# Kernel tuning notes

Measured on AMD Instinct MI355X. Metric: run time of the kernel, lower is better.

## Reference

```python
import jax, jax.numpy as jnp
import numpy as np

B, N, DIM = 2, 2048, 1024
H, DH = 16, 64
INNER = H * DH            # 1024
FF_INNER = 4 * DIM        # 4096
EPS = 1e-5


def _layer_norm(x, g, b):
    mu = jnp.mean(x, axis=-1, keepdims=True)
    var = jnp.mean(jnp.square(x - mu), axis=-1, keepdims=True)
    return (x - mu) * jax.lax.rsqrt(var + EPS) * g + b


def _self_attention(x, wq, wk, wv, wo, bo):
    # wq/wk/wv: [INNER, DIM] (torch Linear layout, y = x @ W^T)
    b, n, _ = x.shape
    q = jnp.einsum('bnd,id->bni', x, wq).reshape(b, n, H, DH).transpose(0, 2, 1, 3)
    k = jnp.einsum('bnd,id->bni', x, wk).reshape(b, n, H, DH).transpose(0, 2, 1, 3)
    v = jnp.einsum('bnd,id->bni', x, wv).reshape(b, n, H, DH).transpose(0, 2, 1, 3)
    scale = DH ** -0.5
    sim = jnp.einsum('bhid,bhjd->bhij', q, k) * scale   # [B,H,N,N]
    attn = jax.nn.softmax(sim, axis=-1)
    out = jnp.einsum('bhij,bhjd->bhid', attn, v)
    out = out.transpose(0, 2, 1, 3).reshape(b, n, INNER)
    return jnp.einsum('bni,di->bnd', out, wo) + bo


def _geglu_ff(x, w1, b1, w2, b2):
    # w1: [2*FF_INNER, DIM], w2: [DIM, FF_INNER]
    h = jnp.einsum('bnd,id->bni', x, w1) + b1
    a, gate = jnp.split(h, 2, axis=-1)
    h = a * jax.nn.gelu(gate, approximate=False)
    return jnp.einsum('bni,di->bnd', h, w2) + b2


def setup_inputs() -> dict:
    key = jax.random.key(0)
    ks = jax.random.split(key, 12)
    s = 0.02
    inp = {
        'x': jax.random.normal(ks[0], (B, N, DIM), jnp.float32),
        'ln1_g': jnp.ones((DIM,), jnp.float32),
        'ln1_b': jnp.zeros((DIM,), jnp.float32),
        'w_q1': jax.random.normal(ks[1], (INNER, DIM), jnp.float32) * s,
        'w_k1': jax.random.normal(ks[2], (INNER, DIM), jnp.float32) * s,
        'w_v1': jax.random.normal(ks[3], (INNER, DIM), jnp.float32) * s,
        'w_o1': jax.random.normal(ks[4], (DIM, INNER), jnp.float32) * s,
        'b_o1': jnp.zeros((DIM,), jnp.float32),
        'ln2_g': jnp.ones((DIM,), jnp.float32),
        'ln2_b': jnp.zeros((DIM,), jnp.float32),
        'w_q2': jax.random.normal(ks[5], (INNER, DIM), jnp.float32) * s,
        'w_k2': jax.random.normal(ks[6], (INNER, DIM), jnp.float32) * s,
        'w_v2': jax.random.normal(ks[7], (INNER, DIM), jnp.float32) * s,
        'w_o2': jax.random.normal(ks[8], (DIM, INNER), jnp.float32) * s,
        'b_o2': jnp.zeros((DIM,), jnp.float32),
        'ln3_g': jnp.ones((DIM,), jnp.float32),
        'ln3_b': jnp.zeros((DIM,), jnp.float32),
        'w_ff1': jax.random.normal(ks[9], (2 * FF_INNER, DIM), jnp.float32) * s,
        'b_ff1': jnp.zeros((2 * FF_INNER,), jnp.float32),
        'w_ff2': jax.random.normal(ks[10], (DIM, FF_INNER), jnp.float32) * s,
        'b_ff2': jnp.zeros((DIM,), jnp.float32),
    }
    return inp


def reference(x, ln1_g, ln1_b, w_q1, w_k1, w_v1, w_o1, b_o1,
              ln2_g, ln2_b, w_q2, w_k2, w_v2, w_o2, b_o2,
              ln3_g, ln3_b, w_ff1, b_ff1, w_ff2, b_ff2):
    # attn1 (self) + residual
    x = _self_attention(_layer_norm(x, ln1_g, ln1_b), w_q1, w_k1, w_v1, w_o1, b_o1) + x
    # attn2 (self, context=None) + residual
    x = _self_attention(_layer_norm(x, ln2_g, ln2_b), w_q2, w_k2, w_v2, w_o2, b_o2) + x
    # GEGLU feed-forward + residual
    x = _geglu_ff(_layer_norm(x, ln3_g, ln3_b), w_ff1, b_ff1, w_ff2, b_ff2) + x
    return x
```

## Files before the change

### kernel.cpp

```cpp
#include <hip/hip_runtime.h>
#include <hip/hip_bf16.h>

using bf16x8 = __attribute__((ext_vector_type(8))) short;
using f32x4  = __attribute__((ext_vector_type(4))) float;
using f32x16 = __attribute__((ext_vector_type(16))) float;
typedef unsigned int u32;
typedef unsigned short u16;
using u32x4 = __attribute__((ext_vector_type(4))) u32;

__device__ __forceinline__ u16 f2b(float f) {
  union { float f; u32 u; } v; v.f = f;
  return (u16)((v.u + 0x7FFFu + ((v.u >> 16) & 1u)) >> 16);
}

__device__ __forceinline__ u32 cvtpk(float lo, float hi) {
  u32 r;
  asm("v_cvt_pk_bf16_f32 %0, %1, %2" : "=v"(r) : "v"(lo), "v"(hi));
  return r;
}

__device__ __forceinline__ float exp2_raw(float x) {
  float r;
  asm("v_exp_f32 %0, %1" : "=v"(r) : "v"(x));
  return r;
}

__device__ __forceinline__ void gload16(const void* g, void* l) {
  __builtin_amdgcn_global_load_lds((const __attribute__((address_space(1))) u32*)g,
                                   (__attribute__((address_space(3))) u32*)l, 16, 0, 0);
}

__device__ __forceinline__ float gelu_fast(float x) {
  const float x2 = x * x;
  const float t = x * fmaf(0.044715f, x2, 1.f);
  const float u = exp2f(2.3022080f * t);
  return x * u * __builtin_amdgcn_rcpf(u + 1.f);
}

__global__ __launch_bounds__(256) void castall(
    const float* __restrict__ wq1, const float* __restrict__ wk1,
    const float* __restrict__ wv1, const float* __restrict__ wo1,
    const float* __restrict__ wq2, const float* __restrict__ wk2,
    const float* __restrict__ wv2, const float* __restrict__ wo2,
    const float* __restrict__ wff1, const float* __restrict__ wff2,
    u16* __restrict__ qkv1, u16* __restrict__ o1,
    u16* __restrict__ qkv2, u16* __restrict__ o2,
    u16* __restrict__ ff1p, u16* __restrict__ ff2) {
  const long e = ((long)blockIdx.x * 256 + threadIdx.x) * 4;
  constexpr long M1 = 1l << 20;
  const float* s; u16* d;
  if (e < 3 * M1) {
    s = (e < M1 ? wq1 + e : (e < 2 * M1 ? wk1 + (e - M1) : wv1 + (e - 2 * M1)));
    d = qkv1 + e;
  } else if (e < 4 * M1) {
    s = wo1 + (e - 3 * M1); d = o1 + (e - 3 * M1);
  } else if (e < 7 * M1) {
    long r = e - 4 * M1;
    s = (r < M1 ? wq2 + r : (r < 2 * M1 ? wk2 + (r - M1) : wv2 + (r - 2 * M1)));
    d = qkv2 + r;
  } else if (e < 8 * M1) {
    s = wo2 + (e - 7 * M1); d = o2 + (e - 7 * M1);
  } else if (e < 16 * M1) {
    long r = e - 8 * M1;
    long p = r >> 10, col = r & 1023;
    long g = p >> 5, rr = p & 31;
    long lr = (rr < 16) ? (g << 4) + rr : 4096 + (g << 4) + (rr - 16);
    s = wff1 + (lr << 10) + col; d = ff1p + r;
  } else {
    long r = e - 16 * M1;
    s = wff2 + r; d = ff2 + r;
  }
  float4 v = *(const float4*)s;
  ushort4 o;
  o.x = f2b(v.x); o.y = f2b(v.y); o.z = f2b(v.z); o.w = f2b(v.w);
  *(ushort4*)d = o;
}

__global__ __launch_bounds__(256) void ln_kernel(const float* __restrict__ x,
                                                 const float* __restrict__ g,
                                                 const float* __restrict__ b,
                                                 u16* __restrict__ y) {
  const int row = blockIdx.x;
  const int t = threadIdx.x;
  const float* xr = x + (size_t)row * 1024;
  float4 v = ((const float4*)xr)[t];
  float s  = v.x + v.y + v.z + v.w;
  float s2 = v.x * v.x + v.y * v.y + v.z * v.z + v.w * v.w;
  #pragma unroll
  for (int m = 1; m < 64; m <<= 1) {
    s  += __shfl_xor(s, m);
    s2 += __shfl_xor(s2, m);
  }
  __shared__ float red[8];
  if ((t & 63) == 0) { red[(t >> 6) * 2] = s; red[(t >> 6) * 2 + 1] = s2; }
  __syncthreads();
  s  = red[0] + red[2] + red[4] + red[6];
  s2 = red[1] + red[3] + red[5] + red[7];
  const float mu = s * (1.f / 1024.f);
  const float var = s2 * (1.f / 1024.f) - mu * mu;
  const float rs = rsqrtf(var + 1e-5f);
  float4 gv = ((const float4*)g)[t];
  float4 bv = ((const float4*)b)[t];
  ushort4 o;
  o.x = f2b((v.x - mu) * rs * gv.x + bv.x);
  o.y = f2b((v.y - mu) * rs * gv.y + bv.y);
  o.z = f2b((v.z - mu) * rs * gv.z + bv.z);
  o.w = f2b((v.w - mu) * rs * gv.w + bv.w);
  ((ushort4*)(y + (size_t)row * 1024))[t] = o;
}

__global__ __launch_bounds__(512, 4) void gemm_out(
    const u16* __restrict__ A, const u16* __restrict__ Bw,
    const float* __restrict__ bias, const float* __restrict__ resid,
    float* __restrict__ out, int N, int K) {
  extern __shared__ u16 lds[];
  const int tid = threadIdx.x;
  const int l = tid & 63, wid = tid >> 6;
  const int li = l & 15, lg = l >> 4;
  const int wr = wid >> 2, wc = wid & 3;
  const int nx = N >> 7;
  const int cpx = gridDim.x >> 3;
  const int v = (blockIdx.x & 7) * cpx + (blockIdx.x >> 3);
  const int by = v / nx, bx = v - by * nx;
  const int m0 = by << 7, n0 = bx << 7;

  const int sr = tid >> 3;
  const int sc = ((tid & 7) ^ (sr & 7)) << 3;
  const int dc = (tid & 7) << 3;
  const int sc0 = (lg * 8) ^ ((li & 7) << 3);
  const int sc1 = sc0 ^ 32;

  f32x4 acc[4][2] = {};

  auto stageA = [&](int kb, int t2) {
    #pragma unroll
    for (int s = 0; s < 2; ++s)
      gload16(A + (size_t)(m0 + s * 64 + sr) * K + t2 * 64 + sc,
              lds + kb * 8192 + (s * 64 + sr) * 64 + dc);
  };
  auto stageB = [&](int kb, int t2) {
    #pragma unroll
    for (int s = 0; s < 2; ++s)
      gload16(Bw + (size_t)(n0 + s * 64 + sr) * K + t2 * 64 + sc,
              lds + 16384 + kb * 8192 + (s * 64 + sr) * 64 + dc);
  };

  const int NT = K >> 6;
  stageA(0, 0); stageB(0, 0);
  __builtin_amdgcn_sched_barrier(0);
  stageA(1, 1); stageB(1, 1);
  __builtin_amdgcn_sched_barrier(0);
  asm volatile("s_waitcnt vmcnt(4)" ::: "memory");
  __builtin_amdgcn_s_barrier();
  __builtin_amdgcn_sched_barrier(0);

  for (int t = 0; t < NT; ++t) {
    const int kb = t & 1;
    const u16* Ab = lds + kb * 8192 + (wr * 64 + li) * 64;
    const u16* Bb = lds + 16384 + kb * 8192 + (wc * 32 + li) * 64;
    bf16x8 a[4], b[2];

    #pragma unroll
    for (int mi = 0; mi < 4; ++mi) a[mi] = *(const bf16x8*)(Ab + mi * 1024 + sc0);
    #pragma unroll
    for (int n = 0; n < 2; ++n)  b[n]  = *(const bf16x8*)(Bb + n * 1024 + sc0);
    __builtin_amdgcn_s_barrier();
    __builtin_amdgcn_s_setprio(1);
    #pragma unroll
    for (int mi = 0; mi < 4; ++mi)
      #pragma unroll
      for (int n = 0; n < 2; ++n)
        acc[mi][n] = __builtin_amdgcn_mfma_f32_16x16x32_bf16(a[mi], b[n], acc[mi][n], 0, 0, 0);
    __builtin_amdgcn_s_setprio(0);
    __builtin_amdgcn_s_barrier();

    #pragma unroll
    for (int mi = 0; mi < 4; ++mi) a[mi] = *(const bf16x8*)(Ab + mi * 1024 + sc1);
    #pragma unroll
    for (int n = 0; n < 2; ++n)  b[n]  = *(const bf16x8*)(Bb + n * 1024 + sc1);
    __builtin_amdgcn_s_barrier();
    __builtin_amdgcn_s_setprio(1);
    #pragma unroll
    for (int mi = 0; mi < 4; ++mi)
      #pragma unroll
      for (int n = 0; n < 2; ++n)
        acc[mi][n] = __builtin_amdgcn_mfma_f32_16x16x32_bf16(a[mi], b[n], acc[mi][n], 0, 0, 0);
    __builtin_amdgcn_s_setprio(0);
    if (t + 2 < NT) {
      stageA(kb, t + 2); stageB(kb, t + 2);
      asm volatile("s_waitcnt vmcnt(4)" ::: "memory");
    } else if (t + 2 == NT) {
      asm volatile("s_waitcnt vmcnt(0)" ::: "memory");
    }
    __builtin_amdgcn_s_barrier();
    __builtin_amdgcn_sched_barrier(0);
  }

  #pragma unroll
  for (int mi = 0; mi < 4; ++mi) {
    const int m = m0 + wr * 64 + mi * 16 + lg * 4;
    #pragma unroll
    for (int n = 0; n < 2; ++n) {
      const int j = n0 + wc * 32 + n * 16 + li;
      const float bj = bias[j];
      #pragma unroll
      for (int rb = 0; rb < 4; ++rb)
        out[(size_t)(m + rb) * N + j] =
            acc[mi][n][rb] + bj + resid[(size_t)(m + rb) * N + j];
    }
  }
}

#define KLOOP_PROLOGUE()                                                      \
  stageA(0, 0); stageB(0, 0); stageA(1, 0); stageB(1, 0);                     \
  __builtin_amdgcn_sched_barrier(0);                                          \
  stageA(0, 1); stageB(0, 1);                                                 \
  __builtin_amdgcn_sched_barrier(0);                                          \
  asm volatile("s_waitcnt vmcnt(4)" ::: "memory");                            \
  __builtin_amdgcn_s_barrier();                                               \
  __builtin_amdgcn_sched_barrier(0);

#define KLOOP_BODY(NT)                                                        \
  bf16x8 b0[4], b1[4];                                                        \
  for (int t = 0; t < NT; ++t) {                                              \
    const int kb = t & 1;                                                     \
    const u16* Abase0 = lds + (kb * 2 + 0) * 8192 + rowA0;                    \
    const u16* Abase1 = lds + (kb * 2 + 1) * 8192 + rowA0;                    \
    const u16* Bbase  = lds + (kb * 2 + bhn) * 8192 + rowB0;                  \
    bf16x8 a[4];                                                              \
                                                      \
    _Pragma("unroll")                                                         \
    for (int j = 0; j < 4; ++j) a[j]  = *(const bf16x8*)(Abase0 + j * 1024 + sc0); \
    _Pragma("unroll")                                                         \
    for (int n = 0; n < 4; ++n) b0[n] = *(const bf16x8*)(Bbase + n * 1024 + sc0); \
    if (t + 1 < NT) stageA(1, t + 1);                                         \
    __builtin_amdgcn_s_setprio(1);                                            \
    _Pragma("unroll")                                                         \
    for (int j = 0; j < 4; ++j)                                               \
      _Pragma("unroll")                                                       \
      for (int n = 0; n < 4; ++n)                                             \
        acc[j][n] = __builtin_amdgcn_mfma_f32_16x16x32_bf16(a[j], b0[n], acc[j][n], 0, 0, 0); \
    __builtin_amdgcn_s_setprio(0);                                            \
    __builtin_amdgcn_s_barrier();                                             \
                                                      \
    _Pragma("unroll")                                                         \
    for (int j = 0; j < 4; ++j) a[j]  = *(const bf16x8*)(Abase0 + j * 1024 + sc1); \
    _Pragma("unroll")                                                         \
    for (int n = 0; n < 4; ++n) b1[n] = *(const bf16x8*)(Bbase + n * 1024 + sc1); \
    if (t + 1 < NT) stageB(1, t + 1);                                         \
    __builtin_amdgcn_s_setprio(1);                                            \
    _Pragma("unroll")                                                         \
    for (int j = 0; j < 4; ++j)                                               \
      _Pragma("unroll")                                                       \
      for (int n = 0; n < 4; ++n)                                             \
        acc[j][n] = __builtin_amdgcn_mfma_f32_16x16x32_bf16(a[j], b1[n], acc[j][n], 0, 0, 0); \
    __builtin_amdgcn_s_setprio(0);                                            \
    __builtin_amdgcn_s_barrier();                                             \
                                                      \
    _Pragma("unroll")                                                         \
    for (int j = 0; j < 4; ++j) a[j] = *(const bf16x8*)(Abase1 + j * 1024 + sc0); \
    if (t + 2 < NT) stageA(0, t + 2);                                         \
    __builtin_amdgcn_s_setprio(1);                                            \
    _Pragma("unroll")                                                         \
    for (int j = 0; j < 4; ++j)                                               \
      _Pragma("unroll")                                                       \
      for (int n = 0; n < 4; ++n)                                             \
        acc[4 + j][n] = __builtin_amdgcn_mfma_f32_16x16x32_bf16(a[j], b0[n], acc[4 + j][n], 0, 0, 0); \
    __builtin_amdgcn_s_setprio(0);                                            \
    __builtin_amdgcn_s_barrier();                                             \
                                                      \
    _Pragma("unroll")                                                         \
    for (int j = 0; j < 4; ++j) a[j] = *(const bf16x8*)(Abase1 + j * 1024 + sc1); \
    if (t + 2 < NT) stageB(0, t + 2);                                         \
    __builtin_amdgcn_s_setprio(1);                                            \
    _Pragma("unroll")                                                         \
    for (int j = 0; j < 4; ++j)                                               \
      _Pragma("unroll")                                                       \
      for (int n = 0; n < 4; ++n)                                             \
        acc[4 + j][n] = __builtin_amdgcn_mfma_f32_16x16x32_bf16(a[j], b1[n], acc[4 + j][n], 0, 0, 0); \
    __builtin_amdgcn_s_setprio(0);                                            \
    if (t < NT - 2)       asm volatile("s_waitcnt vmcnt(4)" ::: "memory");    \
    else if (t == NT - 2) asm volatile("s_waitcnt vmcnt(0)" ::: "memory");    \
    __builtin_amdgcn_s_barrier();                                             \
  }

__global__ __launch_bounds__(512, 2) void gemm_ff1(
    const u16* __restrict__ A, const u16* __restrict__ Wp,
    const float* __restrict__ bias, u16* __restrict__ out) {
  extern __shared__ u16 lds[];
  const int tid = threadIdx.x;
  const int l = tid & 63, wid = tid >> 6;
  const int li = l & 15, lg = l >> 4;
  const int wr = wid >> 2, wc = wid & 3;
  const int xcd = blockIdx.x & 7, r = blockIdx.x >> 3;
  const int bx = (xcd & 3) * 8 + (r >> 3);
  const int by = (xcd >> 2) * 8 + (r & 7);

  const int lr8 = l >> 3;
  const int scb = ((l & 7) ^ lr8) << 3;
  const int sc0 = (lg * 8) ^ ((li & 7) << 3);
  const int sc1 = sc0 ^ 32;

  const int rowA0 = (wr * 64 + li) * 64;
  const int rowB0 = 32768 + ((wc & 1) * 64 + li) * 64;
  const int bhn = wc >> 1;

  f32x4 acc[8][4] = {};

  auto stageA = [&](int h, int t2) {
    const int kb2 = t2 & 1;
    #pragma unroll
    for (int s = 0; s < 2; ++s) {
      const u16* g = A + (size_t)(by * 256 + s * 128 + h * 64 + wid * 8 + lr8) * 1024
                       + t2 * 64 + scb;
      u16* d = lds + (kb2 * 2 + h) * 8192 + s * 4096 + wid * 512;
      gload16(g, d);
    }
  };
  auto stageB = [&](int h, int t2) {
    const int kb2 = t2 & 1;
    #pragma unroll
    for (int s = 0; s < 2; ++s) {
      const u16* g = Wp + (size_t)(bx * 256 + h * 128 + s * 64 + wid * 8 + lr8) * 1024
                        + t2 * 64 + scb;
      u16* d = lds + 32768 + (kb2 * 2 + h) * 8192 + s * 4096 + wid * 512;
      gload16(g, d);
    }
  };

  KLOOP_PROLOGUE()
  KLOOP_BODY(16)

  #pragma unroll
  for (int nj = 0; nj < 2; ++nj) {
    const int c = bx * 128 + wc * 32 + nj * 16 + li;
    const float ba = bias[c];
    const float bg = bias[4096 + c];
    #pragma unroll
    for (int mi = 0; mi < 8; ++mi) {
      #pragma unroll
      for (int rb = 0; rb < 4; ++rb) {
        const float av = acc[mi][2 * nj][rb] + ba;
        const float gv = acc[mi][2 * nj + 1][rb] + bg;
        out[(size_t)(by * 256 + wr * 128 + mi * 16 + lg * 4 + rb) * 4096 + c]
            = f2b(av * gelu_fast(gv));
      }
    }
  }
}

__global__ __launch_bounds__(512, 2) void gemm_qkv(
    const u16* __restrict__ A, const u16* __restrict__ Wp,
    u16* __restrict__ outp) {
  extern __shared__ u16 lds[];
  const int tid = threadIdx.x;
  const int l = tid & 63, wid = tid >> 6;
  const int li = l & 15, lg = l >> 4;
  const int wr = wid >> 2, wc = wid & 3;
  const int xcd = blockIdx.x & 7, r = blockIdx.x >> 3;
  const int by = (xcd >> 1) * 4 + r / 6;
  const int bx = (xcd & 1) * 6 + r % 6;

  const int lr8 = l >> 3;
  const int scb = ((l & 7) ^ lr8) << 3;
  const int sc0 = (lg * 8) ^ ((li & 7) << 3);
  const int sc1 = sc0 ^ 32;

  const int rowA0 = (wr * 64 + li) * 64;
  const int rowB0 = 32768 + ((wc & 1) * 64 + li) * 64;
  const int bhn = wc >> 1;

  f32x4 acc[8][4] = {};

  auto stageA = [&](int h, int t2) {
    const int kb2 = t2 & 1;
    #pragma unroll
    for (int s = 0; s < 2; ++s) {
      const u16* g = A + (size_t)(by * 256 + s * 128 + h * 64 + wid * 8 + lr8) * 1024
                       + t2 * 64 + scb;
      u16* d = lds + (kb2 * 2 + h) * 8192 + s * 4096 + wid * 512;
      gload16(g, d);
    }
  };
  auto stageB = [&](int h, int t2) {
    const int kb2 = t2 & 1;
    #pragma unroll
    for (int s = 0; s < 2; ++s) {
      const u16* g = Wp + (size_t)(bx * 256 + h * 128 + s * 64 + wid * 8 + lr8) * 1024
                        + t2 * 64 + scb;
      u16* d = lds + 32768 + (kb2 * 2 + h) * 8192 + s * 4096 + wid * 512;
      gload16(g, d);
    }
  };

  KLOOP_PROLOGUE()
  KLOOP_BODY(16)

  #pragma unroll
  for (int mi = 0; mi < 8; ++mi) {
    const int mbase = by * 256 + wr * 128 + mi * 16 + lg * 4;
    #pragma unroll
    for (int ni = 0; ni < 4; ++ni) {
      const int j = bx * 256 + wc * 64 + ni * 16 + li;
      f32x4 a = acc[mi][ni];
      const int sec = j >> 10, jj = j & 1023;
      const int h = jj >> 6, dd = jj & 63;
      u16* base = outp + (size_t)sec * 4194304;
      if (sec == 0) {
        #pragma unroll
        for (int rb = 0; rb < 4; ++rb) {
          const int m = mbase + rb;
          const int bb = m >> 11, n = m & 2047;
          base[(((size_t)bb * 16 + h) * 2048 + n) * 64 + dd] =
              f2b(a[rb] * 0.18033688011112042f);
        }
      } else if (sec == 1) {
        #pragma unroll
        for (int rb = 0; rb < 4; ++rb) {
          const int m = mbase + rb;
          const int bb = m >> 11, n = m & 2047;
          base[(((size_t)bb * 16 + h) * 2048 + n) * 64 + (dd ^ ((n & 7) << 3))] =
              f2b(a[rb]);
        }
      } else {
        const int bb = mbase >> 11, n = mbase & 2047;
        const int ng = n & ~63, nl = n & 63;
        const int nl2 = (nl & 51) | ((nl & 4) << 1) | ((nl & 8) >> 1);
        const int col = ng | (nl2 ^ ((dd & 7) << 3));
        ushort4 pk;
        pk.x = f2b(a[0]); pk.y = f2b(a[1]); pk.z = f2b(a[2]); pk.w = f2b(a[3]);
        *(ushort4*)&base[(((size_t)bb * 16 + h) * 64 + dd) * 2048 + col] = pk;
      }
    }
  }
}

__global__ __launch_bounds__(256, 2) void attn_fwd(
    const u16* __restrict__ Q, const u16* __restrict__ K,
    const u16* __restrict__ Vt, u16* __restrict__ Out) {
  __shared__ u16 smem[3][8192];
  const int tid = threadIdx.x;
  const int l = tid & 63, w = tid >> 6;
  const int lo = l & 31, hi = l >> 5, l7 = l & 7;
  const int bh = blockIdx.x & 31, qt = blockIdx.x >> 5;
  const int b_ = bh >> 4, h = bh & 15;

  const u16* Qg = Q + ((size_t)bh * 2048 + qt * 128 + w * 32 + lo) * 64;
  const u16* Kg = K + (size_t)bh * 2048 * 64;
  const u16* Vg = Vt + (size_t)bh * 64 * 2048;

  bf16x8 qf[4];
  #pragma unroll
  for (int d = 0; d < 4; ++d) qf[d] = *(const bf16x8*)&Qg[d * 16 + hi * 8];

  f32x16 o0 = {}, o1 = {};
  float lrow = 0.f;

  auto stage = [&](int buf, int jt) {
    #pragma unroll
    for (int i = 0; i < 2; ++i)
      gload16(Kg + (size_t)jt * 4096 + i * 2048 + tid * 8,
              &smem[buf][i * 2048 + w * 512]);
    #pragma unroll
    for (int i = 0; i < 2; ++i)
      gload16(Vg + (size_t)(w * 8 + (l >> 3) + i * 32) * 2048 + jt * 64 + l7 * 8,
              &smem[buf][4096 + i * 2048 + w * 512]);
  };

  __builtin_amdgcn_sched_barrier(0);
  stage(0, 0);
  __builtin_amdgcn_sched_barrier(0);
  stage(1, 1);
  __builtin_amdgcn_sched_barrier(0);

  int cur = 0, pre = 2;
  for (int jt = 0; jt < 32; ++jt) {
    if (jt == 0)      asm volatile("s_waitcnt vmcnt(8)" ::: "memory");
    else if (jt < 31) asm volatile("s_waitcnt vmcnt(4)" ::: "memory");
    else              asm volatile("s_waitcnt vmcnt(0)" ::: "memory");
    __builtin_amdgcn_s_barrier();
    __builtin_amdgcn_sched_barrier(0);
    if (jt + 2 < 32) stage(pre, jt + 2);

    const u16* Kl = &smem[cur][0];
    const u16* Vl = &smem[cur][4096];

    bf16x8 kf[4][2], vf0[4], vf1[4];
    #pragma unroll
    for (int dc = 0; dc < 4; ++dc) {
      const int col = (dc * 16 + hi * 8) ^ (l7 << 3);
      kf[dc][0] = *(const bf16x8*)&Kl[lo * 64 + col];
      kf[dc][1] = *(const bf16x8*)&Kl[(32 + lo) * 64 + col];
      vf0[dc]   = *(const bf16x8*)&Vl[lo * 64 + col];
      vf1[dc]   = *(const bf16x8*)&Vl[(32 + lo) * 64 + col];
    }

    f32x16 st[2] = {};
    __builtin_amdgcn_s_setprio(1);
    #pragma unroll
    for (int dc = 0; dc < 4; ++dc) {
      st[0] = __builtin_amdgcn_mfma_f32_32x32x16_bf16(kf[dc][0], qf[dc], st[0], 0, 0, 0);
      st[1] = __builtin_amdgcn_mfma_f32_32x32x16_bf16(kf[dc][1], qf[dc], st[1], 0, 0, 0);
    }
    __builtin_amdgcn_s_setprio(0);

    float p[32], sm[16];
    #pragma unroll
    for (int r = 0; r < 16; ++r) p[r]      = exp2_raw(st[0][r] - 8.f);
    #pragma unroll
    for (int r = 0; r < 16; ++r) p[16 + r] = exp2_raw(st[1][r] - 8.f);
    #pragma unroll
    for (int r = 0; r < 16; ++r) sm[r] = p[r] + p[16 + r];
    #pragma unroll
    for (int s2 = 8; s2 >= 1; s2 >>= 1)
      #pragma unroll
      for (int r = 0; r < s2; ++r) sm[r] += sm[r + s2];
    lrow += sm[0] + __shfl_xor(sm[0], 32);

    bf16x8 pf[4];
    #pragma unroll
    for (int kp = 0; kp < 4; ++kp) {
      u32x4 wv;
      #pragma unroll
      for (int t2 = 0; t2 < 4; ++t2)
        wv[t2] = cvtpk(p[(kp >> 1) * 16 + (kp & 1) * 8 + t2 * 2],
                       p[(kp >> 1) * 16 + (kp & 1) * 8 + t2 * 2 + 1]);
      union { u32x4 a; bf16x8 b; } cc; cc.a = wv;
      pf[kp] = cc.b;
    }

    __builtin_amdgcn_s_setprio(1);
    #pragma unroll
    for (int kp = 0; kp < 4; ++kp) {
      o0 = __builtin_amdgcn_mfma_f32_32x32x16_bf16(vf0[kp], pf[kp], o0, 0, 0, 0);
      o1 = __builtin_amdgcn_mfma_f32_32x32x16_bf16(vf1[kp], pf[kp], o1, 0, 0, 0);
    }
    __builtin_amdgcn_s_setprio(0);

    cur = (cur == 2) ? 0 : cur + 1;
    pre = (pre == 2) ? 0 : pre + 1;
  }

  const float inv = 1.f / lrow;
  u16* Ob = Out + ((size_t)b_ * 2048 + qt * 128 + w * 32 + lo) * 1024 + h * 64;
  #pragma unroll
  for (int dd = 0; dd < 2; ++dd) {
    #pragma unroll
    for (int R = 0; R < 4; ++R) {
      ushort4 pk;
      const f32x16 oo = dd ? o1 : o0;
      pk.x = f2b(oo[4 * R + 0] * inv); pk.y = f2b(oo[4 * R + 1] * inv);
      pk.z = f2b(oo[4 * R + 2] * inv); pk.w = f2b(oo[4 * R + 3] * inv);
      *(ushort4*)&Ob[dd * 32 + 8 * R + 4 * hi] = pk;
    }
  }
}

extern "C" void kernel_launch(void* const* d_in, const int* in_sizes, int n_in,
                              void* d_out, int out_size, void* d_ws, size_t ws_size,
                              hipStream_t stream) {
  const float* x    = (const float*)d_in[0];
  const float* ln1g = (const float*)d_in[1];
  const float* ln1b = (const float*)d_in[2];
  const float* wq1  = (const float*)d_in[3];
  const float* wk1  = (const float*)d_in[4];
  const float* wv1  = (const float*)d_in[5];
  const float* wo1  = (const float*)d_in[6];
  const float* bo1  = (const float*)d_in[7];
  const float* ln2g = (const float*)d_in[8];
  const float* ln2b = (const float*)d_in[9];
  const float* wq2  = (const float*)d_in[10];
  const float* wk2  = (const float*)d_in[11];
  const float* wv2  = (const float*)d_in[12];
  const float* wo2  = (const float*)d_in[13];
  const float* bo2  = (const float*)d_in[14];
  const float* ln3g = (const float*)d_in[15];
  const float* ln3b = (const float*)d_in[16];
  const float* wff1 = (const float*)d_in[17];
  const float* bff1 = (const float*)d_in[18];
  const float* wff2 = (const float*)d_in[19];
  const float* bff2 = (const float*)d_in[20];

  char* ws = (char*)d_ws;
  const size_t MB = 1024 * 1024;
  u16* wqkv1b = (u16*)(ws + 0 * MB);
  u16* wo1b   = (u16*)(ws + 6 * MB);
  u16* wqkv2b = (u16*)(ws + 8 * MB);
  u16* wo2b   = (u16*)(ws + 14 * MB);
  u16* wff1p  = (u16*)(ws + 16 * MB);
  u16* wff2b  = (u16*)(ws + 32 * MB);
  u16* xn     = (u16*)(ws + 40 * MB);
  u16* Qb     = (u16*)(ws + 48 * MB);
  float* x1   = (float*)(ws + 72 * MB);
  float* x2   = (float*)(ws + 88 * MB);
  u16* hact   = (u16*)(ws + 48 * MB);
  u16* Kb  = Qb + 4194304;
  u16* Vtb = Qb + 8388608;

  hipFuncSetAttribute((const void*)gemm_ff1,
                      hipFuncAttributeMaxDynamicSharedMemorySize, 131072);
  hipFuncSetAttribute((const void*)gemm_qkv,
                      hipFuncAttributeMaxDynamicSharedMemorySize, 131072);
  hipFuncSetAttribute((const void*)gemm_out,
                      hipFuncAttributeMaxDynamicSharedMemorySize, 65536);

  castall<<<20480, 256, 0, stream>>>(wq1, wk1, wv1, wo1, wq2, wk2, wv2, wo2,
                                     wff1, wff2,
                                     wqkv1b, wo1b, wqkv2b, wo2b, wff1p, wff2b);

  ln_kernel<<<4096, 256, 0, stream>>>(x, ln1g, ln1b, xn);
  gemm_qkv<<<192, 512, 131072, stream>>>(xn, wqkv1b, Qb);
  attn_fwd<<<512, 256, 0, stream>>>(Qb, Kb, Vtb, xn);
  gemm_out<<<256, 512, 65536, stream>>>(xn, wo1b, bo1, x, x1, 1024, 1024);

  ln_kernel<<<4096, 256, 0, stream>>>(x1, ln2g, ln2b, xn);
  gemm_qkv<<<192, 512, 131072, stream>>>(xn, wqkv2b, Qb);
  attn_fwd<<<512, 256, 0, stream>>>(Qb, Kb, Vtb, xn);
  gemm_out<<<256, 512, 65536, stream>>>(xn, wo2b, bo2, x1, x2, 1024, 1024);

  ln_kernel<<<4096, 256, 0, stream>>>(x2, ln3g, ln3b, xn);
  gemm_ff1<<<512, 512, 131072, stream>>>(xn, wff1p, bff1, hact);
  gemm_out<<<256, 512, 65536, stream>>>(hact, wff2b, bff2, x2, (float*)d_out, 1024, 4096);
}
```

Baseline: 357.7 us.

## Split attention over two key halves and merge partials in a combine kernel

The attention kernel now splits each (batch, head, query-tile) over two halves of the key sequence. This doubles the grid to 1024 blocks, raises the launch-bounds occupancy target to 4, and shrinks the LDS ring from three buffers to two with full waits. Each half writes unnormalized bf16 partial outputs and row sums to workspace. A new combine kernel adds the two partials, normalizes them and scatters the result into the head-interleaved layout. The aim is better CU occupancy and parallelism. The cost is an extra launch, extra global traffic for the partials, bf16 rounding of the intermediate partials, and a shallower prefetch pipeline.

```diff
diff --git a/kernel.cpp b/kernel.cpp
--- a/kernel.cpp
+++ b/kernel.cpp
@@ -11,6 +11,11 @@
 __device__ __forceinline__ u16 f2b(float f) {
   union { float f; u32 u; } v; v.f = f;
   return (u16)((v.u + 0x7FFFu + ((v.u >> 16) & 1u)) >> 16);
+}
+
+__device__ __forceinline__ float b2f(u16 b) {
+  union { u32 u; float f; } v; v.u = ((u32)b) << 16;
+  return v.f;
 }
 
 __device__ __forceinline__ u32 cvtpk(float lo, float hi) {
@@ -435,15 +440,16 @@
   }
 }
 
-__global__ __launch_bounds__(256, 2) void attn_fwd(
+__global__ __launch_bounds__(256, 4) void attn_split(
     const u16* __restrict__ Q, const u16* __restrict__ K,
-    const u16* __restrict__ Vt, u16* __restrict__ Out) {
-  __shared__ u16 smem[3][8192];
+    const u16* __restrict__ Vt, u16* __restrict__ Op, float* __restrict__ Lp) {
+  __shared__ u16 smem[2][8192];
   const int tid = threadIdx.x;
   const int l = tid & 63, w = tid >> 6;
   const int lo = l & 31, hi = l >> 5, l7 = l & 7;
-  const int bh = blockIdx.x & 31, qt = blockIdx.x >> 5;
-  const int b_ = bh >> 4, h = bh & 15;
+  const int bh = blockIdx.x & 31;
+  const int qt = (blockIdx.x >> 5) & 15;
+  const int kh = blockIdx.x >> 9;
 
   const u16* Qg = Q + ((size_t)bh * 2048 + qt * 128 + w * 32 + lo) * 64;
   const u16* Kg = K + (size_t)bh * 2048 * 64;
@@ -467,20 +473,14 @@
               &smem[buf][4096 + i * 2048 + w * 512]);
   };
 
-  __builtin_amdgcn_sched_barrier(0);
-  stage(0, 0);
-  __builtin_amdgcn_sched_barrier(0);
-  stage(1, 1);
-  __builtin_amdgcn_sched_barrier(0);
-
-  int cur = 0, pre = 2;
-  for (int jt = 0; jt < 32; ++jt) {
-    if (jt == 0)      asm volatile("s_waitcnt vmcnt(8)" ::: "memory");
-    else if (jt < 31) asm volatile("s_waitcnt vmcnt(4)" ::: "memory");
-    else              asm volatile("s_waitcnt vmcnt(0)" ::: "memory");
+  stage(0, kh * 16);
+
+  for (int i = 0; i < 16; ++i) {
+    const int cur = i & 1;
+    asm volatile("s_waitcnt vmcnt(0)" ::: "memory");
     __builtin_amdgcn_s_barrier();
     __builtin_amdgcn_sched_barrier(0);
-    if (jt + 2 < 32) stage(pre, jt + 2);
+    if (i + 1 < 16) stage(cur ^ 1, kh * 16 + i + 1);
 
     const u16* Kl = &smem[cur][0];
     const u16* Vl = &smem[cur][4096];
@@ -536,24 +536,43 @@
       o1 = __builtin_amdgcn_mfma_f32_32x32x16_bf16(vf1[kp], pf[kp], o1, 0, 0, 0);
     }
     __builtin_amdgcn_s_setprio(0);
-
-    cur = (cur == 2) ? 0 : cur + 1;
-    pre = (pre == 2) ? 0 : pre + 1;
-  }
-
-  const float inv = 1.f / lrow;
-  u16* Ob = Out + ((size_t)b_ * 2048 + qt * 128 + w * 32 + lo) * 1024 + h * 64;
+    __builtin_amdgcn_s_barrier();
+  }
+
+  const int row = bh * 2048 + qt * 128 + w * 32 + lo;
+  u16* Ob = Op + (size_t)kh * 4194304 + (size_t)row * 64;
   #pragma unroll
   for (int dd = 0; dd < 2; ++dd) {
     #pragma unroll
     for (int R = 0; R < 4; ++R) {
       ushort4 pk;
       const f32x16 oo = dd ? o1 : o0;
-      pk.x = f2b(oo[4 * R + 0] * inv); pk.y = f2b(oo[4 * R + 1] * inv);
-      pk.z = f2b(oo[4 * R + 2] * inv); pk.w = f2b(oo[4 * R + 3] * inv);
+      pk.x = f2b(oo[4 * R + 0]); pk.y = f2b(oo[4 * R + 1]);
+      pk.z = f2b(oo[4 * R + 2]); pk.w = f2b(oo[4 * R + 3]);
       *(ushort4*)&Ob[dd * 32 + 8 * R + 4 * hi] = pk;
     }
   }
+  if (hi == 0) Lp[kh * 65536 + row] = lrow;
+}
+
+__global__ __launch_bounds__(256) void attn_combine(
+    const u16* __restrict__ Op, const float* __restrict__ Lp,
+    u16* __restrict__ xn) {
+  const int idx = blockIdx.x * 256 + threadIdx.x;
+  const int row = idx >> 3;
+  const int dq  = (idx & 7) * 8;
+  const int bh = row >> 11, n = row & 2047;
+  const int b_ = bh >> 4, h = bh & 15;
+  const float inv = 1.f / (Lp[row] + Lp[65536 + row]);
+  const size_t oa = (size_t)row * 64 + dq;
+  bf16x8 a = *(const bf16x8*)&Op[oa];
+  bf16x8 b = *(const bf16x8*)&Op[4194304 + oa];
+  union { bf16x8 v; u16 e[8]; } ua, ub, uo;
+  ua.v = a; ub.v = b;
+  #pragma unroll
+  for (int j = 0; j < 8; ++j)
+    uo.e[j] = f2b((b2f(ua.e[j]) + b2f(ub.e[j])) * inv);
+  *(bf16x8*)&xn[((size_t)b_ * 2048 + n) * 1024 + h * 64 + dq] = uo.v;
 }
 
 extern "C" void kernel_launch(void* const* d_in, const int* in_sizes, int n_in,
@@ -597,6 +616,11 @@
   u16* Kb  = Qb + 4194304;
   u16* Vtb = Qb + 8388608;
 
+  u16*   Opart1 = (u16*)(ws + 72 * MB);
+  float* Lpart1 = (float*)(ws + 88 * MB);
+  u16*   Opart2 = (u16*)(ws + 88 * MB);
+  float* Lpart2 = (float*)(ws + 0 * MB);
+
   hipFuncSetAttribute((const void*)gemm_ff1,
                       hipFuncAttributeMaxDynamicSharedMemorySize, 131072);
   hipFuncSetAttribute((const void*)gemm_qkv,
@@ -610,12 +634,14 @@
 
   ln_kernel<<<4096, 256, 0, stream>>>(x, ln1g, ln1b, xn);
   gemm_qkv<<<192, 512, 131072, stream>>>(xn, wqkv1b, Qb);
-  attn_fwd<<<512, 256, 0, stream>>>(Qb, Kb, Vtb, xn);
+  attn_split<<<1024, 256, 0, stream>>>(Qb, Kb, Vtb, Opart1, Lpart1);
+  attn_combine<<<2048, 256, 0, stream>>>(Opart1, Lpart1, xn);
   gemm_out<<<256, 512, 65536, stream>>>(xn, wo1b, bo1, x, x1, 1024, 1024);
 
   ln_kernel<<<4096, 256, 0, stream>>>(x1, ln2g, ln2b, xn);
   gemm_qkv<<<192, 512, 131072, stream>>>(xn, wqkv2b, Qb);
-  attn_fwd<<<512, 256, 0, stream>>>(Qb, Kb, Vtb, xn);
+  attn_split<<<1024, 256, 0, stream>>>(Qb, Kb, Vtb, Opart2, Lpart2);
+  attn_combine<<<2048, 256, 0, stream>>>(Opart2, Lpart2, xn);
   gemm_out<<<256, 512, 65536, stream>>>(xn, wo2b, bo2, x1, x2, 1024, 1024);
 
   ln_kernel<<<4096, 256, 0, stream>>>(x2, ln3g, ln3b, xn);
```

Result: slower. 422.2 us (+18.0%).
